# Optimization experiments

Measured on AMD Instinct MI355X. Metric: run time of the kernel, lower is better.

## Reference

```python
import jax, jax.numpy as jnp
import numpy as np


def setup_inputs() -> dict:
    key = jax.random.key(0)
    k1, k2, k3, k4 = jax.random.split(key, 4)
    N, E, DIN, H1, H2 = 100000, 1600000, 128, 64, 32
    x = jax.random.normal(k1, (N, DIN), dtype=jnp.float32)
    edge_index = jax.random.randint(k2, (2, E), 0, N, dtype=jnp.int64)
    # Glorot-style scaled init for the two GCN weight matrices (no bias)
    W1 = jax.random.normal(k3, (DIN, H1), dtype=jnp.float32) * (1.0 / np.sqrt(DIN))
    W2 = jax.random.normal(k4, (H1, H2), dtype=jnp.float32) * (1.0 / np.sqrt(H1))
    return {"x": x, "edge_index": edge_index, "W1": W1, "W2": W2}


def reference(x, edge_index, W1, W2):
    N = x.shape[0]
    loop = jnp.arange(N, dtype=edge_index.dtype)
    src = jnp.concatenate([edge_index[0], loop])  # [E+N]
    dst = jnp.concatenate([edge_index[1], loop])  # [E+N]
    # symmetric GCN normalization with self-loops (edge_weight = 1)
    deg = jax.ops.segment_sum(jnp.ones(src.shape, x.dtype), dst, num_segments=N)
    dinv = jnp.where(deg > 0, jax.lax.rsqrt(deg), 0.0)
    norm = dinv[src] * dinv[dst]  # [E+N]

    def gcn_conv(h, W):
        h = h @ W  # transform first (PyG GCNConv order)
        msg = h[src] * norm[:, None]  # gather + scale
        return jax.ops.segment_sum(msg, dst, num_segments=N)  # scatter-add

    hidden1 = jax.nn.relu(gcn_conv(x, W1))
    z = gcn_conv(hidden1, W2)
    return z
```

## Files before the change

kernel.cpp:

```cpp
#include <hip/hip_runtime.h>
#include <hip/hip_fp16.h>

#define DIN 128
#define H1  64
#define H2  32
#define NCH 512
#define BSH 8

typedef _Float16 f16x8 __attribute__((ext_vector_type(8)));
typedef _Float16 f16x4 __attribute__((ext_vector_type(4)));
typedef float    f32x4 __attribute__((ext_vector_type(4)));

__global__ __launch_bounds__(256) void k_hist(const int* __restrict__ dst,
        int* __restrict__ H, int E, int NB, int chunk) {
    __shared__ int lh[512];
    int c = blockIdx.x, tid = threadIdx.x;
    for (int b = tid; b < NB; b += 256) lh[b] = 0;
    __syncthreads();
    int e0 = c * chunk, e1 = min(E, e0 + chunk);
    for (int e = e0 + tid; e < e1; e += 256)
        atomicAdd(&lh[dst[e] >> BSH], 1);
    __syncthreads();
    for (int b = tid; b < NB; b += 256) H[(size_t)b * NCH + c] = lh[b];
}

__global__ __launch_bounds__(256) void k_scan1(const int* __restrict__ in,
        int* __restrict__ out, int* __restrict__ partial, int N) {
    int tid = threadIdx.x;
    int base = blockIdx.x * 1024 + tid * 4;
    int v0 = (base + 0 < N) ? in[base + 0] : 0;
    int v1 = (base + 1 < N) ? in[base + 1] : 0;
    int v2 = (base + 2 < N) ? in[base + 2] : 0;
    int v3 = (base + 3 < N) ? in[base + 3] : 0;
    int sum = v0 + v1 + v2 + v3;
    int lane = tid & 63, wid = tid >> 6;
    int x = sum;
#pragma unroll
    for (int off = 1; off < 64; off <<= 1) {
        int y = __shfl_up(x, off, 64);
        if (lane >= off) x += y;
    }
    __shared__ int wsum[4];
    if (lane == 63) wsum[wid] = x;
    __syncthreads();
    int wbase = 0;
    for (int w = 0; w < wid; ++w) wbase += wsum[w];
    int excl = wbase + x - sum;
    if (base + 0 < N) out[base + 0] = excl;
    if (base + 1 < N) out[base + 1] = excl + v0;
    if (base + 2 < N) out[base + 2] = excl + v0 + v1;
    if (base + 3 < N) out[base + 3] = excl + v0 + v1 + v2;
    if (tid == 0) partial[blockIdx.x] = wsum[0] + wsum[1] + wsum[2] + wsum[3];
}

__global__ __launch_bounds__(256) void k_scan2(int* __restrict__ partial, int nb) {
    int tid = threadIdx.x;
    int v = (tid < nb) ? partial[tid] : 0;
    __shared__ int tmp[256];
    tmp[tid] = v;
    __syncthreads();
    for (int off = 1; off < 256; off <<= 1) {
        int y = (tid >= off) ? tmp[tid - off] : 0;
        __syncthreads();
        tmp[tid] += y;
        __syncthreads();
    }
    if (tid < nb) partial[tid] = tmp[tid] - v;
}

__global__ void k_scan3b(int* __restrict__ a, const int* __restrict__ partial, int n) {
    int i = blockIdx.x * blockDim.x + threadIdx.x;
    if (i < n) a[i] += partial[i >> 10];
}

__global__ __launch_bounds__(256) void k_bsort(const int* __restrict__ src,
        const int* __restrict__ dst, const int* __restrict__ H,
        int2* __restrict__ ep, int E, int NB, int chunk) {
    __shared__ int cur[512];
    int c = blockIdx.x, tid = threadIdx.x;
    for (int b = tid; b < NB; b += 256) cur[b] = H[(size_t)b * NCH + c];
    __syncthreads();
    int e0 = c * chunk, e1 = min(E, e0 + chunk);
    for (int e = e0 + tid; e < e1; e += 256) {
        int s = src[e], d = dst[e];
        int pos = atomicAdd(&cur[d >> BSH], 1);
        ep[pos] = make_int2(s, d);
    }
}

__global__ __launch_bounds__(256) void k_csr(const int2* __restrict__ ep,
        const int* __restrict__ H, int* __restrict__ degi, int* __restrict__ rowptr,
        float* __restrict__ dinv, int* __restrict__ csr_src, int E, int N, int NB) {
    __shared__ int cnt[256], pos[256], wsum[4];
    int b = blockIdx.x, tid = threadIdx.x;
    int base = b << BSH;
    cnt[tid] = 0;
    int bstart = H[(size_t)b * NCH];
    int bend = (b + 1 < NB) ? H[(size_t)(b + 1) * NCH] : E;
    __syncthreads();
    for (int e = bstart + tid; e < bend; e += 256)
        atomicAdd(&cnt[ep[e].y - base], 1);
    __syncthreads();
    int v = cnt[tid];
    int lane = tid & 63, wid = tid >> 6;
    int x = v;
#pragma unroll
    for (int off = 1; off < 64; off <<= 1) {
        int y = __shfl_up(x, off, 64);
        if (lane >= off) x += y;
    }
    if (lane == 63) wsum[wid] = x;
    __syncthreads();
    int wbase = 0;
    for (int w = 0; w < wid; ++w) wbase += wsum[w];
    int excl = wbase + x - v;
    int n = base + tid;
    if (n < N) {
        degi[n]   = v;
        dinv[n]   = rsqrtf((float)v + 1.0f);
        rowptr[n] = bstart + excl;
    }
    pos[tid] = bstart + excl;
    __syncthreads();
    for (int e = bstart + tid; e < bend; e += 256) {
        int2 p = ep[e];
        int q = atomicAdd(&pos[p.y - base], 1);
        csr_src[q] = p.x;
    }
}

__global__ __launch_bounds__(256) void k_mgemm1(const float* __restrict__ x,
        const float* __restrict__ W1, const float* __restrict__ dinv,
        _Float16* __restrict__ t1h, int N) {
    __shared__ _Float16 sA[64 * 128];
    __shared__ _Float16 sB[64 * 128];
    int tid = threadIdx.x;
    int row0 = blockIdx.x * 64;
#pragma unroll
    for (int i = 0; i < 8; ++i) {
        int idx4 = tid + 256 * i;
        int r = idx4 >> 5, c4 = idx4 & 31;
        int row = row0 + r;
        float4 v = make_float4(0.f, 0.f, 0.f, 0.f);
        if (row < N) v = *(const float4*)&x[(size_t)row * DIN + c4 * 4];
        f16x4 h;
        h[0] = (_Float16)v.x; h[1] = (_Float16)v.y;
        h[2] = (_Float16)v.z; h[3] = (_Float16)v.w;
        int byte = (c4 * 8) ^ ((r & 7) << 4);
        *(f16x4*)((char*)sA + r * 256 + byte) = h;
    }
    {
        int n = tid & 63, kq = tid >> 6;
        _Float16 tmp[32];
#pragma unroll
        for (int kk = 0; kk < 32; ++kk)
            tmp[kk] = (_Float16)W1[(size_t)(kq * 32 + kk) * H1 + n];
#pragma unroll
        for (int j = 0; j < 4; ++j) {
            int byte = ((kq * 32 + j * 8) * 2) ^ ((n & 7) << 4);
            *(f16x8*)((char*)sB + n * 256 + byte) = *(f16x8*)&tmp[j * 8];
        }
    }
    __syncthreads();
    int lane = tid & 63, w = tid >> 6;
    int lr = lane & 15, kg = lane >> 4;
    f32x4 acc[4] = {};
    int ar = w * 16 + lr;
    const char* pa = (const char*)sA + ar * 256;
    int axor = (ar & 7) << 4;
#pragma unroll
    for (int ks = 0; ks < 4; ++ks) {
        int kb = ks * 64 + kg * 16;
        f16x8 a = *(const f16x8*)(pa + (kb ^ axor));
#pragma unroll
        for (int nt = 0; nt < 4; ++nt) {
            int bn = nt * 16 + lr;
            f16x8 b = *(const f16x8*)((const char*)sB + bn * 256 + (kb ^ ((bn & 7) << 4)));
            acc[nt] = __builtin_amdgcn_mfma_f32_16x16x32_f16(a, b, acc[nt], 0, 0, 0);
        }
    }
#pragma unroll
    for (int rg = 0; rg < 4; ++rg) {
        int R = row0 + w * 16 + kg * 4 + rg;
        if (R < N) {
            float dv = dinv[R];
#pragma unroll
            for (int nt = 0; nt < 4; ++nt)
                t1h[(size_t)R * H1 + nt * 16 + lr] = (_Float16)(acc[nt][rg] * dv);
        }
    }
}

__global__ __launch_bounds__(256) void k_mgemm2(const _Float16* __restrict__ aggh,
        const float* __restrict__ W2, const float* __restrict__ dinv,
        _Float16* __restrict__ t2h, int N) {
    __shared__ _Float16 sA[64 * 64];
    __shared__ _Float16 sB[32 * 64];
    int tid = threadIdx.x;
    int row0 = blockIdx.x * 64;
#pragma unroll
    for (int i = 0; i < 2; ++i) {
        int idx8 = tid + 256 * i;
        int r = idx8 >> 3, c8 = idx8 & 7;
        int row = row0 + r;
        f16x8 h = {};
        if (row < N) h = *(const f16x8*)&aggh[(size_t)row * H1 + c8 * 8];
        int byte = (c8 * 16) ^ ((r & 7) << 4);
        *(f16x8*)((char*)sA + r * 128 + byte) = h;
    }
    {
        int n = tid & 31, kq = tid >> 5;
        _Float16 tmp[8];
#pragma unroll
        for (int kk = 0; kk < 8; ++kk)
            tmp[kk] = (_Float16)W2[(size_t)(kq * 8 + kk) * H2 + n];
        int byte = (kq * 16) ^ ((n & 7) << 4);
        *(f16x8*)((char*)sB + n * 128 + byte) = *(f16x8*)&tmp[0];
    }
    __syncthreads();
    int lane = tid & 63, w = tid >> 6;
    int lr = lane & 15, kg = lane >> 4;
    f32x4 acc[2] = {};
    int ar = w * 16 + lr;
    const char* pa = (const char*)sA + ar * 128;
    int axor = (ar & 7) << 4;
#pragma unroll
    for (int ks = 0; ks < 2; ++ks) {
        int kb = ks * 64 + kg * 16;
        f16x8 a = *(const f16x8*)(pa + (kb ^ axor));
#pragma unroll
        for (int nt = 0; nt < 2; ++nt) {
            int bn = nt * 16 + lr;
            f16x8 b = *(const f16x8*)((const char*)sB + bn * 128 + (kb ^ ((bn & 7) << 4)));
            acc[nt] = __builtin_amdgcn_mfma_f32_16x16x32_f16(a, b, acc[nt], 0, 0, 0);
        }
    }
#pragma unroll
    for (int rg = 0; rg < 4; ++rg) {
        int R = row0 + w * 16 + kg * 4 + rg;
        if (R < N) {
            float dv = dinv[R];
#pragma unroll
            for (int nt = 0; nt < 2; ++nt)
                t2h[(size_t)R * H2 + nt * 16 + lr] = (_Float16)(acc[nt][rg] * dv);
        }
    }
}

template <int LOGF2, bool FUSE>
__global__ __launch_bounds__(256) void k_aggh(const int* __restrict__ rowptr,
        const int* __restrict__ degi, const int* __restrict__ csr_src,
        const float* __restrict__ dinv, const __half2* __restrict__ tp,
        void* __restrict__ outv, int N) {
    const int F2 = 1 << LOGF2;
    int local = threadIdx.x >> LOGF2;
    int j = threadIdx.x & (F2 - 1);
    int n = blockIdx.x * (256 >> LOGF2) + local;
    if (n >= N) return;
    int start = rowptr[n];
    int deg = degi[n];
    float2 f = __half22float2(tp[((size_t)n << LOGF2) + j]);
    float ax = f.x, ay = f.y;
    int k = 0;
    for (; k + 4 <= deg; k += 4) {
        int s0 = csr_src[start + k + 0];
        int s1 = csr_src[start + k + 1];
        int s2 = csr_src[start + k + 2];
        int s3 = csr_src[start + k + 3];
        float2 f0 = __half22float2(tp[((size_t)s0 << LOGF2) + j]);
        float2 f1 = __half22float2(tp[((size_t)s1 << LOGF2) + j]);
        float2 f2 = __half22float2(tp[((size_t)s2 << LOGF2) + j]);
        float2 f3 = __half22float2(tp[((size_t)s3 << LOGF2) + j]);
        ax += f0.x + f1.x + f2.x + f3.x;
        ay += f0.y + f1.y + f2.y + f3.y;
    }
    for (; k < deg; ++k) {
        int s = csr_src[start + k];
        float2 f0 = __half22float2(tp[((size_t)s << LOGF2) + j]);
        ax += f0.x; ay += f0.y;
    }
    float dv = dinv[n];
    size_t idx = ((size_t)n << LOGF2) + j;
    if (FUSE) {
        ((__half2*)outv)[idx] =
            __floats2half2_rn(fmaxf(ax * dv, 0.f), fmaxf(ay * dv, 0.f));
    } else {
        ((float2*)outv)[idx] = make_float2(ax * dv, ay * dv);
    }
}

extern "C" void kernel_launch(void* const* d_in, const int* in_sizes, int n_in,
                              void* d_out, int out_size, void* d_ws, size_t ws_size,
                              hipStream_t stream) {
    const float* x  = (const float*)d_in[0];
    const int*   ei = (const int*)d_in[1];
    const float* W1 = (const float*)d_in[2];
    const float* W2 = (const float*)d_in[3];

    const int N = in_sizes[0] / DIN;
    const int E = in_sizes[1] / 2;
    const int* src = ei;
    const int* dst = ei + E;

    const int NB    = (N + (1 << BSH) - 1) >> BSH;
    const int NBNCH = NB * NCH;
    const int chunk = (E + NCH - 1) / NCH;

    float*    dinv    = (float*)d_ws;
    int*      degi    = (int*)(dinv + N);
    int*      rowptr  = degi + N;
    int*      H       = rowptr + N;
    int*      partial = H + NBNCH;
    int*      csr_src = partial + 256;
    _Float16* t1h     = (_Float16*)(csr_src + E);
    _Float16* agg1h   = t1h + (size_t)N * H1;
    _Float16* t2h     = t1h;
    float*    out     = (float*)d_out;
    int2*     ep      = (int2*)t1h;

    k_hist<<<NCH, 256, 0, stream>>>(dst, H, E, NB, chunk);
    k_scan1<<<(NBNCH + 1023) / 1024, 256, 0, stream>>>(H, H, partial, NBNCH);
    k_scan2<<<1, 256, 0, stream>>>(partial, (NBNCH + 1023) / 1024);
    k_scan3b<<<(NBNCH + 255) / 256, 256, 0, stream>>>(H, partial, NBNCH);
    k_bsort<<<NCH, 256, 0, stream>>>(src, dst, H, ep, E, NB, chunk);
    k_csr<<<NB, 256, 0, stream>>>(ep, H, degi, rowptr, dinv, csr_src, E, N, NB);

    const int ntile = (N + 63) / 64;

    k_mgemm1<<<ntile, 256, 0, stream>>>(x, W1, dinv, t1h, N);
    k_aggh<5, true><<<(N + 7) / 8, 256, 0, stream>>>(rowptr, degi, csr_src, dinv,
                                                     (const __half2*)t1h, agg1h, N);

    k_mgemm2<<<ntile, 256, 0, stream>>>(agg1h, W2, dinv, t2h, N);
    k_aggh<4, false><<<(N + 15) / 16, 256, 0, stream>>>(rowptr, degi, csr_src, dinv,
                                                        (const __half2*)t2h, out, N);
}
```

Before: 141.7 us.

## Pack bucketed edges into one int and prefetch CSR indices via shuffles

Bucket sort now stores each edge as one 32-bit word: the source index in the low 20 bits and the destination offset within the bucket in the high bits. This halves the traffic of the temporary edge array. The aggregation kernel loads up to 64 neighbour indices cooperatively across the feature lanes with coalesced loads, then broadcasts them with shuffles, instead of having every lane reload the same indices. The packing assumes N fits in 20 bits, and the shuffle loop with a variable count adds control overhead.

```diff
diff --git a/kernel.cpp b/kernel.cpp
--- a/kernel.cpp
+++ b/kernel.cpp
@@ -75,7 +75,7 @@
 
 __global__ __launch_bounds__(256) void k_bsort(const int* __restrict__ src,
         const int* __restrict__ dst, const int* __restrict__ H,
-        int2* __restrict__ ep, int E, int NB, int chunk) {
+        int* __restrict__ ep, int E, int NB, int chunk) {
     __shared__ int cur[512];
     int c = blockIdx.x, tid = threadIdx.x;
     for (int b = tid; b < NB; b += 256) cur[b] = H[(size_t)b * NCH + c];
@@ -84,11 +84,11 @@
     for (int e = e0 + tid; e < e1; e += 256) {
         int s = src[e], d = dst[e];
         int pos = atomicAdd(&cur[d >> BSH], 1);
-        ep[pos] = make_int2(s, d);
-    }
-}
-
-__global__ __launch_bounds__(256) void k_csr(const int2* __restrict__ ep,
+        ep[pos] = s | ((d & ((1 << BSH) - 1)) << 20);
+    }
+}
+
+__global__ __launch_bounds__(256) void k_csr(const int* __restrict__ ep,
         const int* __restrict__ H, int* __restrict__ degi, int* __restrict__ rowptr,
         float* __restrict__ dinv, int* __restrict__ csr_src, int E, int N, int NB) {
     __shared__ int cnt[256], pos[256], wsum[4];
@@ -99,7 +99,7 @@
     int bend = (b + 1 < NB) ? H[(size_t)(b + 1) * NCH] : E;
     __syncthreads();
     for (int e = bstart + tid; e < bend; e += 256)
-        atomicAdd(&cnt[ep[e].y - base], 1);
+        atomicAdd(&cnt[ep[e] >> 20], 1);
     __syncthreads();
     int v = cnt[tid];
     int lane = tid & 63, wid = tid >> 6;
@@ -123,9 +123,9 @@
     pos[tid] = bstart + excl;
     __syncthreads();
     for (int e = bstart + tid; e < bend; e += 256) {
-        int2 p = ep[e];
-        int q = atomicAdd(&pos[p.y - base], 1);
-        csr_src[q] = p.x;
+        int p = ep[e];
+        int q = atomicAdd(&pos[p >> 20], 1);
+        csr_src[q] = p & 0xFFFFF;
     }
 }
 
@@ -248,11 +248,12 @@
 }
 
 template <int LOGF2, bool FUSE>
-__global__ __launch_bounds__(256) void k_aggh(const int* __restrict__ rowptr,
+__global__ __launch_bounds__(256) void k_aggs(const int* __restrict__ rowptr,
         const int* __restrict__ degi, const int* __restrict__ csr_src,
         const float* __restrict__ dinv, const __half2* __restrict__ tp,
         void* __restrict__ outv, int N) {
-    const int F2 = 1 << LOGF2;
+    const int F2  = 1 << LOGF2;
+    const int PRE = 64 >> LOGF2;
     int local = threadIdx.x >> LOGF2;
     int j = threadIdx.x & (F2 - 1);
     int n = blockIdx.x * (256 >> LOGF2) + local;
@@ -261,23 +262,28 @@
     int deg = degi[n];
     float2 f = __half22float2(tp[((size_t)n << LOGF2) + j]);
     float ax = f.x, ay = f.y;
+    int pre[PRE];
+#pragma unroll
+    for (int u = 0; u < PRE; ++u)
+        pre[u] = (u * F2 + j < deg) ? csr_src[start + u * F2 + j] : 0;
+    int kcap = min(deg, 64);
     int k = 0;
-    for (; k + 4 <= deg; k += 4) {
-        int s0 = csr_src[start + k + 0];
-        int s1 = csr_src[start + k + 1];
-        int s2 = csr_src[start + k + 2];
-        int s3 = csr_src[start + k + 3];
-        float2 f0 = __half22float2(tp[((size_t)s0 << LOGF2) + j]);
-        float2 f1 = __half22float2(tp[((size_t)s1 << LOGF2) + j]);
-        float2 f2 = __half22float2(tp[((size_t)s2 << LOGF2) + j]);
-        float2 f3 = __half22float2(tp[((size_t)s3 << LOGF2) + j]);
-        ax += f0.x + f1.x + f2.x + f3.x;
-        ay += f0.y + f1.y + f2.y + f3.y;
+#pragma unroll
+    for (int u = 0; u < PRE; ++u) {
+        if (k >= kcap) break;
+        int cnt = min(kcap - k, F2);
+#pragma unroll 8
+        for (int t = 0; t < cnt; ++t) {
+            int s = __shfl(pre[u], t, F2);
+            float2 g = __half22float2(tp[((size_t)s << LOGF2) + j]);
+            ax += g.x; ay += g.y;
+        }
+        k += F2;
     }
     for (; k < deg; ++k) {
         int s = csr_src[start + k];
-        float2 f0 = __half22float2(tp[((size_t)s << LOGF2) + j]);
-        ax += f0.x; ay += f0.y;
+        float2 g = __half22float2(tp[((size_t)s << LOGF2) + j]);
+        ax += g.x; ay += g.y;
     }
     float dv = dinv[n];
     size_t idx = ((size_t)n << LOGF2) + j;
@@ -316,7 +322,7 @@
     _Float16* agg1h   = t1h + (size_t)N * H1;
     _Float16* t2h     = t1h;
     float*    out     = (float*)d_out;
-    int2*     ep      = (int2*)t1h;
+    int*      ep      = (int*)t1h;
 
     k_hist<<<NCH, 256, 0, stream>>>(dst, H, E, NB, chunk);
     k_scan1<<<(NBNCH + 1023) / 1024, 256, 0, stream>>>(H, H, partial, NBNCH);
@@ -328,10 +334,10 @@
     const int ntile = (N + 63) / 64;
 
     k_mgemm1<<<ntile, 256, 0, stream>>>(x, W1, dinv, t1h, N);
-    k_aggh<5, true><<<(N + 7) / 8, 256, 0, stream>>>(rowptr, degi, csr_src, dinv,
+    k_aggs<5, true><<<(N + 7) / 8, 256, 0, stream>>>(rowptr, degi, csr_src, dinv,
                                                      (const __half2*)t1h, agg1h, N);
 
     k_mgemm2<<<ntile, 256, 0, stream>>>(agg1h, W2, dinv, t2h, N);
-    k_aggh<4, false><<<(N + 15) / 16, 256, 0, stream>>>(rowptr, degi, csr_src, dinv,
+    k_aggs<4, false><<<(N + 15) / 16, 256, 0, stream>>>(rowptr, degi, csr_src, dinv,
                                                         (const __half2*)t2h, out, N);
 }
```

After: 166.2 us. 1.17x slower.
